# Performance work log

Hardware: AMD Instinct MI355X
Metric: run time of the kernel (lower is better)

## Reference

```python
import jax, jax.numpy as jnp
import numpy as np

DIM = 768
HEADS = 12
HEAD_DIM = DIM // HEADS
EPS = 1e-5


def setup_inputs() -> dict:
    key = jax.random.key(0)
    ks = jax.random.split(key, 9)
    s = 0.02
    x = jax.random.normal(ks[0], (4, 1024, DIM), dtype=jnp.float32)
    return {
        "x": x,
        "Wqkv_c": jax.random.normal(ks[1], (DIM, 3 * DIM), jnp.float32) * s,
        "bqkv_c": jnp.zeros((3 * DIM,), jnp.float32),
        "Wp_c": jax.random.normal(ks[2], (DIM, DIM), jnp.float32) * s,
        "bp_c": jnp.zeros((DIM,), jnp.float32),
        "Wqkv_ac": jax.random.normal(ks[3], (DIM, 3 * DIM), jnp.float32) * s,
        "bqkv_ac": jnp.zeros((3 * DIM,), jnp.float32),
        "Wp_ac": jax.random.normal(ks[4], (DIM, DIM), jnp.float32) * s,
        "bp_ac": jnp.zeros((DIM,), jnp.float32),
        "gamma": jnp.ones((DIM,), jnp.float32),
        "beta": jnp.zeros((DIM,), jnp.float32),
    }


def _branch(x, Wqkv, bqkv, Wp, bp, causal: bool):
    B, T, C = x.shape
    qkv = (x @ Wqkv + bqkv).reshape(B, T, 3, HEADS, HEAD_DIM)
    qkv = jnp.transpose(qkv, (2, 0, 3, 1, 4))  # [3,B,H,T,Dh]
    q, k, v = qkv[0], qkv[1], qkv[2]
    scores = jnp.einsum("bhqd,bhkd->bhqk", q, k) / np.sqrt(HEAD_DIM).astype(np.float32)
    i = jnp.arange(T)[:, None]
    j = jnp.arange(T)[None, :]
    mask = (j <= i) if causal else (j >= i)  # tril / triu (incl. diagonal)
    scores = jnp.where(mask[None, None], scores, -jnp.inf)
    attn = jax.nn.softmax(scores, axis=-1)
    out = jnp.einsum("bhqk,bhkd->bhqd", attn, v)
    out = jnp.transpose(out, (0, 2, 1, 3)).reshape(B, T, C)
    return out @ Wp + bp


def reference(x, Wqkv_c, bqkv_c, Wp_c, bp_c, Wqkv_ac, bqkv_ac, Wp_ac, bp_ac, gamma, beta):
    out_c = _branch(x, Wqkv_c, bqkv_c, Wp_c, bp_c, causal=True)
    out_ac = _branch(x, Wqkv_ac, bqkv_ac, Wp_ac, bp_ac, causal=False)
    y = x + out_c + out_ac  # residual; dropout is identity at eval
    mu = jnp.mean(y, axis=-1, keepdims=True)
    var = jnp.var(y, axis=-1, keepdims=True)
    return (y - mu) * jax.lax.rsqrt(var + EPS) * gamma + beta
```

## Files before the change

### kernel.cpp

```cpp
#include <hip/hip_runtime.h>
#include <stdint.h>

#define DIM 768
#define HEADS 12
#define HD 64
#define BATCH 4
#define SEQ 1024
#define NTOK (BATCH*SEQ)
#define QKVW (3*DIM)
#define QKW (2*DIM)
#define EPS 1e-5f

typedef __attribute__((ext_vector_type(8))) short short8;
typedef __attribute__((ext_vector_type(4))) float f32x4;

__device__ __forceinline__ unsigned short f2bf(float f) {
    union { float f; unsigned u; } v; v.f = f;
    unsigned r = v.u + 0x7fffu + ((v.u >> 16) & 1u);
    return (unsigned short)(r >> 16);
}
__device__ __forceinline__ float b2f(unsigned short s) {
    union { unsigned u; float f; } v; v.u = (unsigned)s << 16; return v.f;
}

__device__ __forceinline__ void gld_lds16(const void* g, void* l) {
    auto gp = reinterpret_cast<const __attribute__((address_space(1))) unsigned int*>(
        (uintptr_t)g);
    auto lp = reinterpret_cast<__attribute__((address_space(3))) unsigned int*>(
        (unsigned int)(uintptr_t)l);
    __builtin_amdgcn_global_load_lds(gp, lp, 16, 0, 0);
}

#define CVT_X_BLOCKS (NTOK*DIM/1024)
#define CVT_WQ_TILES ((QKVW/32)*(DIM/32))
#define CVT_WP_TILES ((DIM/32)*(DIM/32))
__global__ __launch_bounds__(256) void cvt_all_kernel(
    const float* __restrict__ x,
    const float* __restrict__ Wq0, const float* __restrict__ Wq1,
    const float* __restrict__ Wp0, const float* __restrict__ Wp1,
    unsigned short* __restrict__ xb,
    unsigned short* __restrict__ WqT0, unsigned short* __restrict__ WqT1,
    unsigned short* __restrict__ WpT0, unsigned short* __restrict__ WpT1)
{
    const int bid = blockIdx.x, tid = threadIdx.x;
    if (bid < CVT_X_BLOCKS) {
        const int i = bid * 256 + tid;
        const float4 v = ((const float4*)x)[i];
        ushort4 o4;
        o4.x = f2bf(v.x); o4.y = f2bf(v.y); o4.z = f2bf(v.z); o4.w = f2bf(v.w);
        ((ushort4*)xb)[i] = o4;
        return;
    }
    __shared__ float t[32][33];
    const float* W; unsigned short* WT; int N, K, tile;
    int w = bid - CVT_X_BLOCKS;
    if (w < 2 * CVT_WQ_TILES) {
        const int z = w / CVT_WQ_TILES; tile = w % CVT_WQ_TILES;
        W = z ? Wq1 : Wq0; WT = z ? WqT1 : WqT0; N = QKVW; K = DIM;
    } else {
        w -= 2 * CVT_WQ_TILES;
        const int z = w / CVT_WP_TILES; tile = w % CVT_WP_TILES;
        W = z ? Wp1 : Wp0; WT = z ? WpT1 : WpT0; N = DIM; K = DIM;
    }
    const int ntiles = N / 32;
    const int n0 = (tile % ntiles) * 32, k0 = (tile / ntiles) * 32;
    const int c = tid & 31, rr = tid >> 5;
#pragma unroll
    for (int i = 0; i < 4; ++i)
        t[rr + 8 * i][c] = W[(size_t)(k0 + rr + 8 * i) * N + n0 + c];
    __syncthreads();
#pragma unroll
    for (int i = 0; i < 4; ++i)
        WT[(size_t)(n0 + rr + 8 * i) * K + k0 + c] = f2bf(t[c][rr + 8 * i]);
}

__global__ __launch_bounds__(256) void gemm_qkv_kernel(
    const unsigned short* __restrict__ A,
    const unsigned short* __restrict__ BT0, const unsigned short* __restrict__ BT1,
    const float* __restrict__ bias0, const float* __restrict__ bias1,
    unsigned short* __restrict__ QK0, unsigned short* __restrict__ QK1,
    unsigned short* __restrict__ VT0, unsigned short* __restrict__ VT1)
{
    const int z = blockIdx.z;
    const unsigned short* __restrict__ BT = z ? BT1 : BT0;
    const float* __restrict__ bias = z ? bias1 : bias0;
    unsigned short* __restrict__ QK = z ? QK1 : QK0;
    unsigned short* __restrict__ VT = z ? VT1 : VT0;
    const int K = DIM;

    __shared__ __align__(16) unsigned short sh[17408];
    const int tid = threadIdx.x, lane = tid & 63, wv = tid >> 6;
    const int m0 = blockIdx.y * 128, n0 = blockIdx.x * 128;
    const int wr = wv >> 1, wc = wv & 1;
    const int fm = lane & 15, fk = (lane >> 4) * 8;
    const int c0 = wv * 2;
    const int arow = c0 * 16 + (lane >> 2), kk = (lane & 3) * 8;

    const unsigned short* Ag0 = A  + (size_t)(m0 + arow)      * K + kk;
    const unsigned short* Ag1 = A  + (size_t)(m0 + arow + 16) * K + kk;
    const unsigned short* Bg0 = BT + (size_t)(n0 + arow)      * K + kk;
    const unsigned short* Bg1 = BT + (size_t)(n0 + arow + 16) * K + kk;

    f32x4 acc[4][4];
#pragma unroll
    for (int i = 0; i < 4; ++i)
#pragma unroll
        for (int j = 0; j < 4; ++j) acc[i][j] = f32x4{0.f, 0.f, 0.f, 0.f};

    gld_lds16(Ag0, &sh[c0 * 512]);
    gld_lds16(Ag1, &sh[c0 * 512 + 512]);
    gld_lds16(Bg0, &sh[4096 + c0 * 512]);
    gld_lds16(Bg1, &sh[4096 + c0 * 512 + 512]);

    const int NK = K / 32;
    for (int kt = 0; kt < NK; ++kt) {
        const int p = kt & 1;
        __syncthreads();
        if (kt + 1 < NK) {
            const int off = (kt + 1) * 32;
            const int q = (p ^ 1) * 8192;
            gld_lds16(Ag0 + off, &sh[q + c0 * 512]);
            gld_lds16(Ag1 + off, &sh[q + c0 * 512 + 512]);
            gld_lds16(Bg0 + off, &sh[q + 4096 + c0 * 512]);
            gld_lds16(Bg1 + off, &sh[q + 4096 + c0 * 512 + 512]);
        }
        const int pb = p * 8192;
        short8 af[4], bf[4];
#pragma unroll
        for (int i = 0; i < 4; ++i)
            af[i] = *(const short8*)&sh[pb + (wr * 64 + i * 16 + fm) * 32 + fk];
#pragma unroll
        for (int j = 0; j < 4; ++j)
            bf[j] = *(const short8*)&sh[pb + 4096 + (wc * 64 + j * 16 + fm) * 32 + fk];
#pragma unroll
        for (int i = 0; i < 4; ++i)
#pragma unroll
            for (int j = 0; j < 4; ++j)
                acc[i][j] = __builtin_amdgcn_mfma_f32_16x16x32_bf16(af[i], bf[j], acc[i][j], 0, 0, 0);
    }

    __syncthreads();
    const int rbase = (lane >> 4) * 4;
    const int rowg = tid >> 4, lseg = tid & 15;
    if (n0 < QKW) {
        const float qsc = (n0 < DIM) ? 0.125f : 1.0f;
#pragma unroll
        for (int i = 0; i < 4; ++i) {
            const int ml = wr * 64 + i * 16 + rbase;
#pragma unroll
            for (int j = 0; j < 4; ++j) {
                const int nl = wc * 64 + j * 16 + fm;
                const float bs = bias[n0 + nl];
#pragma unroll
                for (int r = 0; r < 4; ++r)
                    sh[(ml + r) * 136 + nl] = f2bf((acc[i][j][r] + bs) * qsc);
            }
        }
        __syncthreads();
#pragma unroll
        for (int pp = 0; pp < 8; ++pp) {
            const int row = pp * 16 + rowg;
            const uint4 v = *(const uint4*)&sh[row * 136 + lseg * 8];
            *(uint4*)(QK + (size_t)(m0 + row) * QKW + n0 + lseg * 8) = v;
        }
    } else {
        const int b = m0 >> 10, t0 = m0 & 1023;
#pragma unroll
        for (int i = 0; i < 4; ++i) {
            const int tl = wr * 64 + i * 16 + rbase;
#pragma unroll
            for (int j = 0; j < 4; ++j) {
                const int nl = wc * 64 + j * 16 + fm;
                const float bs = bias[n0 + nl];
                const unsigned p0 = f2bf(acc[i][j][0] + bs);
                const unsigned p1 = f2bf(acc[i][j][1] + bs);
                const unsigned p2 = f2bf(acc[i][j][2] + bs);
                const unsigned p3 = f2bf(acc[i][j][3] + bs);
                uint2 u; u.x = p0 | (p1 << 16); u.y = p2 | (p3 << 16);
                *(uint2*)(&sh[nl * 136 + tl]) = u;
            }
        }
        __syncthreads();
#pragma unroll
        for (int pp = 0; pp < 8; ++pp) {
            const int nl = pp * 16 + rowg;
            const int nh = (n0 - QKW) + nl;
            const uint4 v = *(const uint4*)&sh[nl * 136 + lseg * 8];
            *(uint4*)(VT + ((size_t)((b * HEADS + (nh >> 6)) * HD + (nh & 63))) * SEQ
                      + t0 + lseg * 8) = v;
        }
    }
}

__global__ __launch_bounds__(256) void gemm_proj_kernel(
    const unsigned short* __restrict__ A0, const unsigned short* __restrict__ BT0,
    const unsigned short* __restrict__ A1, const unsigned short* __restrict__ BT1,
    const float* __restrict__ b0, const float* __restrict__ b1,
    const float* __restrict__ xres, float* __restrict__ Y0,
    unsigned short* __restrict__ Y1)
{
    const int z = blockIdx.z;
    const unsigned short* __restrict__ A  = z ? A1 : A0;
    const unsigned short* __restrict__ BT = z ? BT1 : BT0;
    __shared__ __align__(16) unsigned short Als[2][64 * 32];
    __shared__ __align__(16) unsigned short Bls[2][128 * 32];
    const int tid = threadIdx.x, lane = tid & 63, wv = tid >> 6;
    const int m0 = blockIdx.y * 64, n0 = blockIdx.x * 128;
    const int fm = lane & 15, fg = lane >> 4, fk = (lane >> 4) * 8;
    const int srw = lane >> 2, kk = (lane & 3) * 8;
    const int K = DIM;

    const unsigned short* Ag  = A  + (size_t)(m0 + wv * 16 + srw) * K + kk;
    const unsigned short* Bg0 = BT + (size_t)(n0 + wv * 32 + srw) * K + kk;
    const unsigned short* Bg1 = BT + (size_t)(n0 + wv * 32 + 16 + srw) * K + kk;

    f32x4 acc[4][2];
#pragma unroll
    for (int i = 0; i < 4; ++i)
#pragma unroll
        for (int j = 0; j < 2; ++j) acc[i][j] = f32x4{0.f, 0.f, 0.f, 0.f};

    gld_lds16(Ag,  &Als[0][wv * 512]);
    gld_lds16(Bg0, &Bls[0][wv * 1024]);
    gld_lds16(Bg1, &Bls[0][wv * 1024 + 512]);

    const int NK = K / 32;
    for (int kt = 0; kt < NK; ++kt) {
        const int p = kt & 1;
        __syncthreads();
        if (kt + 1 < NK) {
            const int off = (kt + 1) * 32;
            gld_lds16(Ag + off,  &Als[p ^ 1][wv * 512]);
            gld_lds16(Bg0 + off, &Bls[p ^ 1][wv * 1024]);
            gld_lds16(Bg1 + off, &Bls[p ^ 1][wv * 1024 + 512]);
        }
        short8 af[4], bf[2];
#pragma unroll
        for (int i = 0; i < 4; ++i)
            af[i] = *(const short8*)&Als[p][(i * 16 + fm) * 32 + fk];
#pragma unroll
        for (int j = 0; j < 2; ++j)
            bf[j] = *(const short8*)&Bls[p][(wv * 32 + j * 16 + fm) * 32 + fk];
#pragma unroll
        for (int i = 0; i < 4; ++i)
#pragma unroll
            for (int j = 0; j < 2; ++j)
                acc[i][j] = __builtin_amdgcn_mfma_f32_16x16x32_bf16(af[i], bf[j], acc[i][j], 0, 0, 0);
    }
#pragma unroll
    for (int i = 0; i < 4; ++i) {
        const int m = m0 + i * 16 + fg * 4;
#pragma unroll
        for (int j = 0; j < 2; ++j) {
            const int n = n0 + wv * 32 + j * 16 + fm;
            if (z == 0) {
                const float bs = b0[n] + b1[n];
#pragma unroll
                for (int r = 0; r < 4; ++r) {
                    const size_t idx = (size_t)(m + r) * DIM + n;
                    Y0[idx] = acc[i][j][r] + xres[idx] + bs;
                }
            } else {
#pragma unroll
                for (int r = 0; r < 4; ++r)
                    Y1[(size_t)(m + r) * DIM + n] = f2bf(acc[i][j][r]);
            }
        }
    }
}

#define KP 72
__global__ __launch_bounds__(256, 3) void attn_fused_kernel(
    const unsigned short* __restrict__ qk_c, const unsigned short* __restrict__ vT_c,
    const unsigned short* __restrict__ qk_ac, const unsigned short* __restrict__ vT_ac,
    unsigned short* __restrict__ o_c, unsigned short* __restrict__ o_ac)
{
    __shared__ __align__(16) unsigned short Kls[2][64 * KP];
    __shared__ __align__(16) unsigned short Vls[2][64 * KP];
    __shared__ __align__(16) unsigned short Ps[4][16 * KP];
    const int tid = threadIdx.x, lane = tid & 63, w = tid >> 6;
    const int fm = lane & 15, fg = lane >> 4;
    const int bh = blockIdx.x, qt = blockIdx.y;
    const int b = bh / HEADS, h = bh % HEADS;
    unsigned short* Psw = &Ps[w][0];
    const int srow = tid >> 3, sseg = (tid & 7) * 8;

    for (int br = 0; br < 2; ++br) {
        const int causal = (br == 0);
        const unsigned short* __restrict__ qk = causal ? qk_c : qk_ac;
        const unsigned short* __restrict__ vT = causal ? vT_c : vT_ac;
        unsigned short* __restrict__ o = causal ? o_c : o_ac;
        const unsigned short* qbase = qk + (size_t)b * SEQ * QKW + h * HD;
        const unsigned short* kbase = qbase + DIM;
        const unsigned short* vtb   = vT + (size_t)(b * HEADS + h) * HD * SEQ;

        short8 qb0, qb1;
        {
            const size_t qoff = (size_t)(qt * 64 + w * 16 + fm) * QKW + fg * 8;
            qb0 = *(const short8*)(qbase + qoff);
            qb1 = *(const short8*)(qbase + qoff + 32);
        }

        float ls = 0.f;
        f32x4 accO[4];
#pragma unroll
        for (int dj = 0; dj < 4; ++dj) accO[dj] = f32x4{0.f, 0.f, 0.f, 0.f};

        const int ktb = causal ? 0 : qt;
        const int kte = causal ? qt : (SEQ / 64 - 1);

        uint4 kr0 = *(const uint4*)(kbase + (size_t)(ktb * 64 + srow) * QKW + sseg);
        uint4 kr1 = *(const uint4*)(kbase + (size_t)(ktb * 64 + srow + 32) * QKW + sseg);
        uint4 vr0 = *(const uint4*)(vtb + (size_t)srow * SEQ + ktb * 64 + sseg);
        uint4 vr1 = *(const uint4*)(vtb + (size_t)(srow + 32) * SEQ + ktb * 64 + sseg);

        if (br) __syncthreads();
        int p = 0;
        for (int kt = ktb; kt <= kte; ++kt) {
            *(uint4*)(&Kls[p][srow * KP + sseg])        = kr0;
            *(uint4*)(&Kls[p][(srow + 32) * KP + sseg]) = kr1;
            *(uint4*)(&Vls[p][srow * KP + sseg])        = vr0;
            *(uint4*)(&Vls[p][(srow + 32) * KP + sseg]) = vr1;
            if (kt < kte) {
                const int ktn = kt + 1;
                kr0 = *(const uint4*)(kbase + (size_t)(ktn * 64 + srow) * QKW + sseg);
                kr1 = *(const uint4*)(kbase + (size_t)(ktn * 64 + srow + 32) * QKW + sseg);
                vr0 = *(const uint4*)(vtb + (size_t)srow * SEQ + ktn * 64 + sseg);
                vr1 = *(const uint4*)(vtb + (size_t)(srow + 32) * SEQ + ktn * 64 + sseg);
            }
            __syncthreads();

            f32x4 st[4];
#pragma unroll
            for (int kj = 0; kj < 4; ++kj) {
                const short8 ka0 = *(const short8*)&Kls[p][(kj * 16 + fm) * KP + fg * 8];
                const short8 ka1 = *(const short8*)&Kls[p][(kj * 16 + fm) * KP + 32 + fg * 8];
                st[kj] = __builtin_amdgcn_mfma_f32_16x16x32_bf16(ka0, qb0, f32x4{0.f,0.f,0.f,0.f}, 0, 0, 0);
                st[kj] = __builtin_amdgcn_mfma_f32_16x16x32_bf16(ka1, qb1, st[kj], 0, 0, 0);
            }
            const bool diag = (kt == qt);
#pragma unroll
            for (int kj = 0; kj < 4; ++kj) {
                float e[4];
#pragma unroll
                for (int r = 0; r < 4; ++r) {
                    float v = st[kj][r];
                    if (diag) {
                        const int ki = kj * 16 + fg * 4 + r;
                        const int qi = w * 16 + fm;
                        const bool ok = causal ? (ki <= qi) : (ki >= qi);
                        if (!ok) v = -1e30f;
                    }
                    e[r] = __expf(v);
                    ls += e[r];
                }
                const unsigned p0 = f2bf(e[0]);
                const unsigned p1 = f2bf(e[1]);
                const unsigned p2 = f2bf(e[2]);
                const unsigned p3 = f2bf(e[3]);
                uint2 u; u.x = p0 | (p1 << 16); u.y = p2 | (p3 << 16);
                *(uint2*)(Psw + fm * KP + kj * 16 + fg * 4) = u;
            }
            const short8 ap0 = *(const short8*)(Psw + fm * KP + fg * 8);
            const short8 ap1 = *(const short8*)(Psw + fm * KP + 32 + fg * 8);
#pragma unroll
            for (int dj = 0; dj < 4; ++dj) {
                const short8 vb0 = *(const short8*)&Vls[p][(dj * 16 + fm) * KP + fg * 8];
                const short8 vb1 = *(const short8*)&Vls[p][(dj * 16 + fm) * KP + 32 + fg * 8];
                accO[dj] = __builtin_amdgcn_mfma_f32_16x16x32_bf16(ap0, vb0, accO[dj], 0, 0, 0);
                accO[dj] = __builtin_amdgcn_mfma_f32_16x16x32_bf16(ap1, vb1, accO[dj], 0, 0, 0);
            }
            p ^= 1;
        }

        float lt = ls;
        lt += __shfl_xor(lt, 16);
        lt += __shfl_xor(lt, 32);
        float li_o[4];
#pragma unroll
        for (int r = 0; r < 4; ++r) li_o[r] = __shfl(lt, fg * 4 + r);
#pragma unroll
        for (int r = 0; r < 4; ++r) {
            const float inv = 1.f / li_o[r];
            const int q = qt * 64 + w * 16 + fg * 4 + r;
            unsigned short* orow = o + ((size_t)b * SEQ + q) * DIM + h * HD;
#pragma unroll
            for (int dj = 0; dj < 4; ++dj)
                orow[dj * 16 + fm] = f2bf(accO[dj][r] * inv);
        }
    }
}

__global__ __launch_bounds__(256) void ln_kernel(
    const float* __restrict__ Y0, const unsigned short* __restrict__ Y1,
    const float* __restrict__ gamma, const float* __restrict__ beta,
    float* __restrict__ out)
{
    const int row = blockIdx.x;
    const int tid = threadIdx.x;
    const float* y0r = Y0 + (size_t)row * DIM;
    const unsigned short* y1r = Y1 + (size_t)row * DIM;
    float v0 = y0r[tid]       + b2f(y1r[tid]);
    float v1 = y0r[tid + 256] + b2f(y1r[tid + 256]);
    float v2 = y0r[tid + 512] + b2f(y1r[tid + 512]);
    float s = v0 + v1 + v2;
    float q = v0 * v0 + v1 * v1 + v2 * v2;
#pragma unroll
    for (int off = 32; off > 0; off >>= 1) {
        s += __shfl_down(s, off);
        q += __shfl_down(q, off);
    }
    __shared__ float rs_[4], rq_[4];
    const int wv = tid >> 6;
    if ((tid & 63) == 0) { rs_[wv] = s; rq_[wv] = q; }
    __syncthreads();
    const float ts = rs_[0] + rs_[1] + rs_[2] + rs_[3];
    const float tq = rq_[0] + rq_[1] + rq_[2] + rq_[3];
    const float mu = ts * (1.f / DIM);
    const float var = tq * (1.f / DIM) - mu * mu;
    const float rstd = rsqrtf(var + EPS);
    out[(size_t)row * DIM + tid]       = (v0 - mu) * rstd * gamma[tid]       + beta[tid];
    out[(size_t)row * DIM + tid + 256] = (v1 - mu) * rstd * gamma[tid + 256] + beta[tid + 256];
    out[(size_t)row * DIM + tid + 512] = (v2 - mu) * rstd * gamma[tid + 512] + beta[tid + 512];
}

extern "C" void kernel_launch(void* const* d_in, const int* in_sizes, int n_in,
                              void* d_out, int out_size, void* d_ws, size_t ws_size,
                              hipStream_t stream)
{
    const float* x       = (const float*)d_in[0];
    const float* Wqkv_c  = (const float*)d_in[1];
    const float* bqkv_c  = (const float*)d_in[2];
    const float* Wp_c    = (const float*)d_in[3];
    const float* bp_c    = (const float*)d_in[4];
    const float* Wqkv_ac = (const float*)d_in[5];
    const float* bqkv_ac = (const float*)d_in[6];
    const float* Wp_ac   = (const float*)d_in[7];
    const float* bp_ac   = (const float*)d_in[8];
    const float* gamma   = (const float*)d_in[9];
    const float* beta    = (const float*)d_in[10];
    float* out = (float*)d_out;

    char* p = (char*)d_ws;
    unsigned short* qk_c   = (unsigned short*)p; p += (size_t)NTOK * QKW * 2;
    unsigned short* qk_ac  = (unsigned short*)p; p += (size_t)NTOK * QKW * 2;
    unsigned short* vT_c   = (unsigned short*)p; p += (size_t)NTOK * DIM * 2;
    unsigned short* vT_ac  = (unsigned short*)p; p += (size_t)NTOK * DIM * 2;
    unsigned short* o_ac   = (unsigned short*)p; p += (size_t)NTOK * DIM * 2;
    unsigned short* xb     = (unsigned short*)p; p += (size_t)NTOK * DIM * 2;
    unsigned short* WqT_c  = (unsigned short*)p; p += (size_t)QKVW * DIM * 2;
    unsigned short* WqT_ac = (unsigned short*)p; p += (size_t)QKVW * DIM * 2;
    unsigned short* WpT_c  = (unsigned short*)p; p += (size_t)DIM * DIM * 2;
    unsigned short* WpT_ac = (unsigned short*)p; p += (size_t)DIM * DIM * 2;
    unsigned short* o_c = WqT_c;
    float*          Y0  = (float*)qk_c;
    unsigned short* Y1  = vT_c;

    cvt_all_kernel<<<CVT_X_BLOCKS + 2 * CVT_WQ_TILES + 2 * CVT_WP_TILES, 256, 0, stream>>>(
        x, Wqkv_c, Wqkv_ac, Wp_c, Wp_ac, xb, WqT_c, WqT_ac, WpT_c, WpT_ac);

    gemm_qkv_kernel<<<dim3(QKVW / 128, NTOK / 128, 2), 256, 0, stream>>>(
        xb, WqT_c, WqT_ac, bqkv_c, bqkv_ac, qk_c, qk_ac, vT_c, vT_ac);

    attn_fused_kernel<<<dim3(BATCH * HEADS, SEQ / 64), 256, 0, stream>>>(
        qk_c, vT_c, qk_ac, vT_ac, o_c, o_ac);

    gemm_proj_kernel<<<dim3(DIM / 128, NTOK / 64, 2), 256, 0, stream>>>(
        o_c, WpT_c, o_ac, WpT_ac, bp_c, bp_ac, x, Y0, Y1);
    ln_kernel<<<NTOK, 256, 0, stream>>>(Y0, Y1, gamma, beta, out);
}
```

Before: 199.9 us.

## Replace direct global-to-LDS loads with register-staged padded LDS tiles and swizzle QKV grid

Both GEMM kernels stop using global_load_lds. They now prefetch the next K-slice into registers and store it into LDS tiles padded to a 36-element row stride, which is meant to reduce LDS bank conflicts on the MFMA fragment reads. The QKV GEMM uses a flattened 1D grid with a remapping of block index to tile, intended to improve L2 locality across XCDs. Each x-conversion thread now handles four float4s. The cost is extra VGPRs and an added barrier per K iteration.

```diff
diff --git a/kernel.cpp b/kernel.cpp
--- a/kernel.cpp
+++ b/kernel.cpp
@@ -23,15 +23,7 @@
     union { unsigned u; float f; } v; v.u = (unsigned)s << 16; return v.f;
 }
 
-__device__ __forceinline__ void gld_lds16(const void* g, void* l) {
-    auto gp = reinterpret_cast<const __attribute__((address_space(1))) unsigned int*>(
-        (uintptr_t)g);
-    auto lp = reinterpret_cast<__attribute__((address_space(3))) unsigned int*>(
-        (unsigned int)(uintptr_t)l);
-    __builtin_amdgcn_global_load_lds(gp, lp, 16, 0, 0);
-}
-
-#define CVT_X_BLOCKS (NTOK*DIM/1024)
+#define CVT_X_BLOCKS (NTOK*DIM/4096)
 #define CVT_WQ_TILES ((QKVW/32)*(DIM/32))
 #define CVT_WP_TILES ((DIM/32)*(DIM/32))
 __global__ __launch_bounds__(256) void cvt_all_kernel(
@@ -44,11 +36,14 @@
 {
     const int bid = blockIdx.x, tid = threadIdx.x;
     if (bid < CVT_X_BLOCKS) {
-        const int i = bid * 256 + tid;
-        const float4 v = ((const float4*)x)[i];
-        ushort4 o4;
-        o4.x = f2bf(v.x); o4.y = f2bf(v.y); o4.z = f2bf(v.z); o4.w = f2bf(v.w);
-        ((ushort4*)xb)[i] = o4;
+        const int base = bid * 1024 + tid;
+#pragma unroll
+        for (int u = 0; u < 4; ++u) {
+            const float4 v = ((const float4*)x)[base + u * 256];
+            ushort4 o4;
+            o4.x = f2bf(v.x); o4.y = f2bf(v.y); o4.z = f2bf(v.z); o4.w = f2bf(v.w);
+            ((ushort4*)xb)[base + u * 256] = o4;
+        }
         return;
     }
     __shared__ float t[32][33];
@@ -74,6 +69,7 @@
         WT[(size_t)(n0 + rr + 8 * i) * K + k0 + c] = f2bf(t[c][rr + 8 * i]);
 }
 
+#define QP 36
 __global__ __launch_bounds__(256) void gemm_qkv_kernel(
     const unsigned short* __restrict__ A,
     const unsigned short* __restrict__ BT0, const unsigned short* __restrict__ BT1,
@@ -81,25 +77,29 @@
     unsigned short* __restrict__ QK0, unsigned short* __restrict__ QK1,
     unsigned short* __restrict__ VT0, unsigned short* __restrict__ VT1)
 {
-    const int z = blockIdx.z;
+    const int gid = blockIdx.x;
+    const int g = gid & 7, t = gid >> 3;
+    const int bx = (g & 1) * 9 + t % 9;
+    const int by = ((g >> 1) & 1) * 16 + t / 9;
+    const int z = g >> 2;
     const unsigned short* __restrict__ BT = z ? BT1 : BT0;
     const float* __restrict__ bias = z ? bias1 : bias0;
     unsigned short* __restrict__ QK = z ? QK1 : QK0;
     unsigned short* __restrict__ VT = z ? VT1 : VT0;
     const int K = DIM;
-
-    __shared__ __align__(16) unsigned short sh[17408];
+    const int m0 = by * 128, n0 = bx * 128;
+
+    __shared__ __align__(16) unsigned short sh[18432];
     const int tid = threadIdx.x, lane = tid & 63, wv = tid >> 6;
-    const int m0 = blockIdx.y * 128, n0 = blockIdx.x * 128;
     const int wr = wv >> 1, wc = wv & 1;
     const int fm = lane & 15, fk = (lane >> 4) * 8;
-    const int c0 = wv * 2;
-    const int arow = c0 * 16 + (lane >> 2), kk = (lane & 3) * 8;
-
-    const unsigned short* Ag0 = A  + (size_t)(m0 + arow)      * K + kk;
-    const unsigned short* Ag1 = A  + (size_t)(m0 + arow + 16) * K + kk;
-    const unsigned short* Bg0 = BT + (size_t)(n0 + arow)      * K + kk;
-    const unsigned short* Bg1 = BT + (size_t)(n0 + arow + 16) * K + kk;
+    const int sr = wv * 32 + (lane >> 2);
+    const int ck = (lane & 3) * 8;
+
+    const unsigned short* Ag0 = A  + (size_t)(m0 + sr)      * K + ck;
+    const unsigned short* Ag1 = A  + (size_t)(m0 + sr + 16) * K + ck;
+    const unsigned short* Bg0 = BT + (size_t)(n0 + sr)      * K + ck;
+    const unsigned short* Bg1 = BT + (size_t)(n0 + sr + 16) * K + ck;
 
     f32x4 acc[4][4];
 #pragma unroll
@@ -107,39 +107,37 @@
 #pragma unroll
         for (int j = 0; j < 4; ++j) acc[i][j] = f32x4{0.f, 0.f, 0.f, 0.f};
 
-    gld_lds16(Ag0, &sh[c0 * 512]);
-    gld_lds16(Ag1, &sh[c0 * 512 + 512]);
-    gld_lds16(Bg0, &sh[4096 + c0 * 512]);
-    gld_lds16(Bg1, &sh[4096 + c0 * 512 + 512]);
+    uint4 a0 = *(const uint4*)Ag0, a1 = *(const uint4*)Ag1;
+    uint4 b0 = *(const uint4*)Bg0, b1 = *(const uint4*)Bg1;
 
     const int NK = K / 32;
     for (int kt = 0; kt < NK; ++kt) {
-        const int p = kt & 1;
-        __syncthreads();
+        const int pb = (kt & 1) * 9216;
+        *(uint4*)&sh[pb + sr * QP + ck]               = a0;
+        *(uint4*)&sh[pb + (sr + 16) * QP + ck]        = a1;
+        *(uint4*)&sh[pb + 4608 + sr * QP + ck]        = b0;
+        *(uint4*)&sh[pb + 4608 + (sr + 16) * QP + ck] = b1;
         if (kt + 1 < NK) {
             const int off = (kt + 1) * 32;
-            const int q = (p ^ 1) * 8192;
-            gld_lds16(Ag0 + off, &sh[q + c0 * 512]);
-            gld_lds16(Ag1 + off, &sh[q + c0 * 512 + 512]);
-            gld_lds16(Bg0 + off, &sh[q + 4096 + c0 * 512]);
-            gld_lds16(Bg1 + off, &sh[q + 4096 + c0 * 512 + 512]);
-        }
-        const int pb = p * 8192;
+            a0 = *(const uint4*)(Ag0 + off); a1 = *(const uint4*)(Ag1 + off);
+            b0 = *(const uint4*)(Bg0 + off); b1 = *(const uint4*)(Bg1 + off);
+        }
+        __syncthreads();
         short8 af[4], bf[4];
 #pragma unroll
         for (int i = 0; i < 4; ++i)
-            af[i] = *(const short8*)&sh[pb + (wr * 64 + i * 16 + fm) * 32 + fk];
+            af[i] = *(const short8*)&sh[pb + (wr * 64 + i * 16 + fm) * QP + fk];
 #pragma unroll
         for (int j = 0; j < 4; ++j)
-            bf[j] = *(const short8*)&sh[pb + 4096 + (wc * 64 + j * 16 + fm) * 32 + fk];
+            bf[j] = *(const short8*)&sh[pb + 4608 + (wc * 64 + j * 16 + fm) * QP + fk];
 #pragma unroll
         for (int i = 0; i < 4; ++i)
 #pragma unroll
             for (int j = 0; j < 4; ++j)
                 acc[i][j] = __builtin_amdgcn_mfma_f32_16x16x32_bf16(af[i], bf[j], acc[i][j], 0, 0, 0);
-    }
-
-    __syncthreads();
+        __syncthreads();
+    }
+
     const int rbase = (lane >> 4) * 4;
     const int rowg = tid >> 4, lseg = tid & 15;
     if (n0 < QKW) {
@@ -202,17 +200,20 @@
     const int z = blockIdx.z;
     const unsigned short* __restrict__ A  = z ? A1 : A0;
     const unsigned short* __restrict__ BT = z ? BT1 : BT0;
-    __shared__ __align__(16) unsigned short Als[2][64 * 32];
-    __shared__ __align__(16) unsigned short Bls[2][128 * 32];
+    __shared__ __align__(16) unsigned short shA[2][64 * QP];
+    __shared__ __align__(16) unsigned short shB[2][128 * QP];
     const int tid = threadIdx.x, lane = tid & 63, wv = tid >> 6;
     const int m0 = blockIdx.y * 64, n0 = blockIdx.x * 128;
     const int fm = lane & 15, fg = lane >> 4, fk = (lane >> 4) * 8;
-    const int srw = lane >> 2, kk = (lane & 3) * 8;
+    const int srw = lane >> 2, ck = (lane & 3) * 8;
     const int K = DIM;
 
-    const unsigned short* Ag  = A  + (size_t)(m0 + wv * 16 + srw) * K + kk;
-    const unsigned short* Bg0 = BT + (size_t)(n0 + wv * 32 + srw) * K + kk;
-    const unsigned short* Bg1 = BT + (size_t)(n0 + wv * 32 + 16 + srw) * K + kk;
+    const unsigned short* Ag  = A  + (size_t)(m0 + wv * 16 + srw) * K + ck;
+    const unsigned short* Bg0 = BT + (size_t)(n0 + wv * 32 + srw) * K + ck;
+    const unsigned short* Bg1 = BT + (size_t)(n0 + wv * 32 + 16 + srw) * K + ck;
+    const int sa = (wv * 16 + srw) * QP + ck;
+    const int sb0 = (wv * 32 + srw) * QP + ck;
+    const int sb1 = (wv * 32 + 16 + srw) * QP + ck;
 
     f32x4 acc[4][2];
 #pragma unroll
@@ -220,32 +221,35 @@
 #pragma unroll
         for (int j = 0; j < 2; ++j) acc[i][j] = f32x4{0.f, 0.f, 0.f, 0.f};
 
-    gld_lds16(Ag,  &Als[0][wv * 512]);
-    gld_lds16(Bg0, &Bls[0][wv * 1024]);
-    gld_lds16(Bg1, &Bls[0][wv * 1024 + 512]);
+    uint4 ar = *(const uint4*)Ag;
+    uint4 br0 = *(const uint4*)Bg0, br1 = *(const uint4*)Bg1;
 
     const int NK = K / 32;
     for (int kt = 0; kt < NK; ++kt) {
         const int p = kt & 1;
-        __syncthreads();
+        *(uint4*)&shA[p][sa]  = ar;
+        *(uint4*)&shB[p][sb0] = br0;
+        *(uint4*)&shB[p][sb1] = br1;
         if (kt + 1 < NK) {
             const int off = (kt + 1) * 32;
-            gld_lds16(Ag + off,  &Als[p ^ 1][wv * 512]);
-            gld_lds16(Bg0 + off, &Bls[p ^ 1][wv * 1024]);
-            gld_lds16(Bg1 + off, &Bls[p ^ 1][wv * 1024 + 512]);
-        }
+            ar  = *(const uint4*)(Ag + off);
+            br0 = *(const uint4*)(Bg0 + off);
+            br1 = *(const uint4*)(Bg1 + off);
+        }
+        __syncthreads();
         short8 af[4], bf[2];
 #pragma unroll
         for (int i = 0; i < 4; ++i)
-            af[i] = *(const short8*)&Als[p][(i * 16 + fm) * 32 + fk];
+            af[i] = *(const short8*)&shA[p][(i * 16 + fm) * QP + fk];
 #pragma unroll
         for (int j = 0; j < 2; ++j)
-            bf[j] = *(const short8*)&Bls[p][(wv * 32 + j * 16 + fm) * 32 + fk];
+            bf[j] = *(const short8*)&shB[p][(wv * 32 + j * 16 + fm) * QP + fk];
 #pragma unroll
         for (int i = 0; i < 4; ++i)
 #pragma unroll
             for (int j = 0; j < 2; ++j)
                 acc[i][j] = __builtin_amdgcn_mfma_f32_16x16x32_bf16(af[i], bf[j], acc[i][j], 0, 0, 0);
+        __syncthreads();
     }
 #pragma unroll
     for (int i = 0; i < 4; ++i) {
@@ -459,7 +463,7 @@
     cvt_all_kernel<<<CVT_X_BLOCKS + 2 * CVT_WQ_TILES + 2 * CVT_WP_TILES, 256, 0, stream>>>(
         x, Wqkv_c, Wqkv_ac, Wp_c, Wp_ac, xb, WqT_c, WqT_ac, WpT_c, WpT_ac);
 
-    gemm_qkv_kernel<<<dim3(QKVW / 128, NTOK / 128, 2), 256, 0, stream>>>(
+    gemm_qkv_kernel<<<(QKVW / 128) * (NTOK / 128) * 2, 256, 0, stream>>>(
         xb, WqT_c, WqT_ac, bqkv_c, bqkv_ac, qk_c, qk_ac, vT_c, vT_ac);
 
     attn_fused_kernel<<<dim3(BATCH * HEADS, SEQ / 64), 256, 0, stream>>>(
```

Result: no change. 201.6 us (+0.8%).
